# Kernel optimization log

Hardware: AMD Instinct MI355X
Metric: run time of the kernel (lower is better)

Reference implementation:

```python
import jax, jax.numpy as jnp
import numpy as np

B, T, H, NH = 4, 1024, 1024, 16
HS = H // NH
FF = 4 * H
EPS = 1e-5


def setup_inputs() -> dict:
    key = jax.random.key(0)
    ks = jax.random.split(key, 12)
    s = 0.02
    inp = {
        "x": jax.random.normal(ks[0], (B, T, H), jnp.float32),
        # attention projections, stored as [in, out] so y = x @ W + b
        "Wq": jax.random.normal(ks[1], (H, H), jnp.float32) * s,
        "bq": jnp.zeros((H,), jnp.float32),
        "Wk": jax.random.normal(ks[2], (H, H), jnp.float32) * s,
        "bk": jnp.zeros((H,), jnp.float32),
        "Wv": jax.random.normal(ks[3], (H, H), jnp.float32) * s,
        "bv": jnp.zeros((H,), jnp.float32),
        "Wo": jax.random.normal(ks[4], (H, H), jnp.float32) * s,
        "bo": jnp.zeros((H,), jnp.float32),
        # layernorms
        "ln1_w": jnp.ones((H,), jnp.float32),
        "ln1_b": jnp.zeros((H,), jnp.float32),
        "ln2_w": jnp.ones((H,), jnp.float32),
        "ln2_b": jnp.zeros((H,), jnp.float32),
        # MLP
        "Wfc": jax.random.normal(ks[5], (H, FF), jnp.float32) * s,
        "bfc": jnp.zeros((FF,), jnp.float32),
        "Wpr": jax.random.normal(ks[6], (FF, H), jnp.float32) * s,
        "bpr": jnp.zeros((H,), jnp.float32),
    }
    return inp


def _layernorm(x, w, b):
    mu = jnp.mean(x, axis=-1, keepdims=True)
    var = jnp.mean(jnp.square(x - mu), axis=-1, keepdims=True)
    return (x - mu) * jax.lax.rsqrt(var + EPS) * w + b


def _rope(x):
    # x: [B, nh, T, hs]; interleaved-pair RoPE, base 10000
    half = HS // 2
    inv_freq = 1.0 / (10000.0 ** (jnp.arange(half, dtype=jnp.float32) / half))
    ang = jnp.arange(T, dtype=jnp.float32)[:, None] * inv_freq[None, :]  # [T, half]
    cos, sin = jnp.cos(ang), jnp.sin(ang)
    xr = x.reshape(*x.shape[:-1], half, 2)
    x0, x1 = xr[..., 0], xr[..., 1]
    r0 = x0 * cos - x1 * sin
    r1 = x0 * sin + x1 * cos
    return jnp.stack([r0, r1], axis=-1).reshape(x.shape)


def _block(x, Wq, bq, Wk, bk, Wv, bv, Wo, bo, ln1_w, ln1_b, ln2_w, ln2_b, Wfc, bfc, Wpr, bpr):
    # --- attention sub-block ---
    h1 = _layernorm(x, ln1_w, ln1_b)
    q = (h1 @ Wq + bq).reshape(B, T, NH, HS).transpose(0, 2, 1, 3)  # [B,nh,T,hs]
    k = (h1 @ Wk + bk).reshape(B, T, NH, HS).transpose(0, 2, 1, 3)
    v = (h1 @ Wv + bv).reshape(B, T, NH, HS).transpose(0, 2, 1, 3)
    q, k = _rope(q), _rope(k)
    scores = jnp.einsum('bhqd,bhkd->bhqk', q, k) / jnp.sqrt(jnp.float32(HS))
    attn = jax.nn.softmax(scores, axis=-1)
    # NOTE: original applies the causal mask AFTER softmax (multiplicative, no renorm)
    causal = jnp.tril(jnp.ones((T, T), jnp.float32))[None, None]
    attn = attn * causal
    out = jnp.einsum('bhqk,bhkd->bhqd', attn, v)
    out = out.transpose(0, 2, 1, 3).reshape(B, T, H)
    x = x + (out @ Wo + bo)
    # --- MLP sub-block ---
    h2 = _layernorm(x, ln2_w, ln2_b)
    m = jax.nn.gelu(h2 @ Wfc + bfc, approximate=False)
    x = x + (m @ Wpr + bpr)
    return x


def reference(x, Wq, bq, Wk, bk, Wv, bv, Wo, bo, ln1_w, ln1_b, ln2_w, ln2_b, Wfc, bfc, Wpr, bpr):
    return _block(x, Wq, bq, Wk, bk, Wv, bv, Wo, bo, ln1_w, ln1_b, ln2_w, ln2_b, Wfc, bfc, Wpr, bpr)
```

## Files before the change

### kernel.cpp

```cpp
#include <hip/hip_runtime.h>
#include <hip/hip_bf16.h>

typedef unsigned short u16;
typedef __attribute__((ext_vector_type(8))) short bf16x8;
typedef __attribute__((ext_vector_type(4))) float f32x4;
typedef __attribute__((ext_vector_type(4))) unsigned short u16x4;

#define B_  4
#define T_  1024
#define H_  1024
#define NH_ 16
#define HS_ 64
#define FF_ 4096
#define M_  (B_*T_)
#define QKV_S 3072

__device__ __forceinline__ u16 f2bf(float f){
  union { float f; unsigned u; } v; v.f = f;
  unsigned r = v.u + 0x7fffu + ((v.u >> 16) & 1u);
  return (u16)(r >> 16);
}
__device__ __forceinline__ float bf2f(u16 h){
  union { unsigned u; float f; } v; v.u = ((unsigned)h) << 16;
  return v.f;
}
__device__ __forceinline__ unsigned pack2bf(float a, float b){
  __hip_bfloat162 h = __float22bfloat162_rn(make_float2(a, b));
  union { __hip_bfloat162 h; unsigned u; } c; c.h = h;
  return c.u;
}

__device__ __forceinline__ void gload_lds16(const void* g, void* l){
  __builtin_amdgcn_global_load_lds(
      (const __attribute__((address_space(1))) unsigned int*)g,
      (__attribute__((address_space(3))) unsigned int*)l,
      16, 0, 0);
}

__device__ __forceinline__ void trans_tile(const float* __restrict__ W,
                                           u16* __restrict__ Wt, int K, int N,
                                           int k0, int n0, int tid)
{
  __shared__ u16 tile[64][68];
  #pragma unroll
  for (int it = 0; it < 4; ++it){
    int ci = tid + it * 256;
    int kr = ci >> 4, nc = ci & 15;
    float4 f = *(const float4*)(W + (size_t)(k0 + kr) * N + n0 + nc * 4);
    tile[kr][nc*4+0] = f2bf(f.x);
    tile[kr][nc*4+1] = f2bf(f.y);
    tile[kr][nc*4+2] = f2bf(f.z);
    tile[kr][nc*4+3] = f2bf(f.w);
  }
  __syncthreads();
  #pragma unroll
  for (int it = 0; it < 4; ++it){
    int co = tid + it * 256;
    int nr = co >> 4, kc = co & 15;
    u16x4 o;
    o[0] = tile[kc*4+0][nr];
    o[1] = tile[kc*4+1][nr];
    o[2] = tile[kc*4+2][nr];
    o[3] = tile[kc*4+3][nr];
    *(u16x4*)(Wt + (size_t)(n0 + nr) * K + k0 + kc * 4) = o;
  }
}

__global__ __launch_bounds__(256) void trans_qkvo_k(
    const float* __restrict__ Wq, const float* __restrict__ Wk,
    const float* __restrict__ Wv, const float* __restrict__ Wo,
    u16* __restrict__ WqkvT, u16* __restrict__ WoT)
{
  const int z = blockIdx.z;
  const float* src = (z == 0) ? Wq : (z == 1) ? Wk : (z == 2) ? Wv : Wo;
  u16* dst = (z == 3) ? WoT : (WqkvT + (size_t)z * 1024 * 1024);
  trans_tile(src, dst, H_, H_, blockIdx.y * 64, blockIdx.x * 64, threadIdx.x);
}

__global__ __launch_bounds__(256) void transpose_cvt(const float* __restrict__ W,
                                                     u16* __restrict__ Wt, int K, int N)
{
  trans_tile(W, Wt, K, N, blockIdx.y * 64, blockIdx.x * 64, threadIdx.x);
}

__global__ __launch_bounds__(256) void vtrans_k(const u16* __restrict__ qkv,
                                                u16* __restrict__ vtg)
{
  __shared__ u16 tile[64][72];
  const int bh = blockIdx.y, tt = blockIdx.x * 64;
  const int b = bh >> 4, h = bh & 15;
  const size_t src = (size_t)b * T_ * QKV_S + h * HS_ + 2048;
  const int tid = threadIdx.x;
  #pragma unroll
  for (int it = 0; it < 2; ++it){
    int ci = tid + it * 256;
    int r = ci >> 3, c = ci & 7;
    bf16x8 vvv = *(const bf16x8*)(qkv + src + (size_t)(tt + r) * QKV_S + c * 8);
    *(bf16x8*)&tile[r][c * 8] = vvv;
  }
  __syncthreads();
  #pragma unroll
  for (int it = 0; it < 2; ++it){
    int co = tid + it * 256;
    int d = co >> 3, c = co & 7;
    bf16x8 ov;
    #pragma unroll
    for (int j = 0; j < 8; ++j) ov[j] = (short)tile[c * 8 + j][d];
    *(bf16x8*)(vtg + (size_t)bh * HS_ * T_ + (size_t)d * T_ + tt + c * 8) = ov;
  }
}

__global__ void prep_small_k(const float* __restrict__ a, const float* __restrict__ b,
                             const float* __restrict__ c, float* __restrict__ o,
                             float* __restrict__ tab){
  int i = blockIdx.x * 256 + threadIdx.x;
  if (i < QKV_S){
    o[i] = (i < 1024) ? a[i] : (i < 2048) ? b[i - 1024] : c[i - 2048];
  } else {
    int j = i - QKV_S;
    if (j < T_ * 32){
      int t = j >> 5, f = j & 31;
      float inv = powf(10000.0f, -(float)f * (1.0f / 32.0f));
      float ang = (float)t * inv;
      tab[j*2+0] = cosf(ang);
      tab[j*2+1] = sinf(ang);
    }
  }
}

__global__ void rope_apply_k(u16* __restrict__ qkv, const float* __restrict__ tab){
  int i = blockIdx.x * blockDim.x + threadIdx.x;
  if (i >= B_*T_*NH_*32) return;
  int pr = i & 31;
  int nh = (i >> 5) & (NH_ - 1);
  int bt = i >> 9;
  int t  = bt & (T_ - 1);
  size_t idx = (size_t)bt * QKV_S + nh * HS_ + pr * 2;
  float c = tab[(t*32 + pr)*2], s = tab[(t*32 + pr)*2 + 1];
  const float qs = 0.125f * 1.44269504f;
  {
    float x0 = bf2f(qkv[idx]), x1 = bf2f(qkv[idx+1]);
    qkv[idx]   = f2bf((x0 * c - x1 * s) * qs);
    qkv[idx+1] = f2bf((x0 * s + x1 * c) * qs);
  }
  {
    float x0 = bf2f(qkv[idx+1024]), x1 = bf2f(qkv[idx+1025]);
    qkv[idx+1024] = f2bf(x0 * c - x1 * s);
    qkv[idx+1025] = f2bf(x0 * s + x1 * c);
  }
}

__global__ __launch_bounds__(256) void ln_kernel(const float* __restrict__ x,
    const float* __restrict__ w, const float* __restrict__ bgain,
    u16* __restrict__ out)
{
  const int row = blockIdx.x;
  const int t = threadIdx.x;
  float4 vv = ((const float4*)(x + (size_t)row * H_))[t];
  float s  = vv.x + vv.y + vv.z + vv.w;
  float s2 = vv.x*vv.x + vv.y*vv.y + vv.z*vv.z + vv.w*vv.w;
  #pragma unroll
  for (int mm = 1; mm < 64; mm <<= 1){ s += __shfl_xor(s, mm); s2 += __shfl_xor(s2, mm); }
  __shared__ float red[8];
  int wid = t >> 6;
  if ((t & 63) == 0){ red[wid] = s; red[4 + wid] = s2; }
  __syncthreads();
  s  = red[0] + red[1] + red[2] + red[3];
  s2 = red[4] + red[5] + red[6] + red[7];
  float mu  = s * (1.0f / H_);
  float var = s2 * (1.0f / H_) - mu * mu;
  float rin = rsqrtf(var + 1e-5f);
  float4 wv = ((const float4*)w)[t];
  float4 bv = ((const float4*)bgain)[t];
  u16x4 ov;
  ov[0] = f2bf((vv.x - mu) * rin * wv.x + bv.x);
  ov[1] = f2bf((vv.y - mu) * rin * wv.y + bv.y);
  ov[2] = f2bf((vv.z - mu) * rin * wv.z + bv.z);
  ov[3] = f2bf((vv.w - mu) * rin * wv.w + bv.w);
  ((u16x4*)(out + (size_t)row * H_))[t] = ov;
}

template<int EPI>
__global__ __launch_bounds__(512, 2) void gemm_big_kernel(
    const u16* __restrict__ A, const u16* __restrict__ Bt,
    const float* __restrict__ bias,
    void* __restrict__ Cout, int M, int N, int K)
{
  __shared__ __attribute__((aligned(16))) u16 As[3][256 * 32];
  __shared__ __attribute__((aligned(16))) u16 Bs[3][256 * 32];
  const int tid  = threadIdx.x;
  const int lane = tid & 63;
  const int wid  = tid >> 6;
  const int wm = wid >> 2, wn = wid & 3;
  const int lrow = lane & 15, lkg = lane >> 4;

  const int gx  = gridDim.x;
  const int nwg = gx * gridDim.y;
  const int wg  = blockIdx.y * gx + blockIdx.x;
  const int nx  = nwg >> 3;
  const int swz = (wg & 7) * nx + (wg >> 3);
  const int m0 = (swz / gx) * 256, n0 = (swz % gx) * 256;

  const int r0 = tid >> 2;
  const int c0 = tid & 3;
  const int s0 = c0 ^ ((r0 >> 1) & 3);
  const u16* Asrc0 = A  + (size_t)(m0 + r0) * K + s0 * 8;
  const u16* Asrc1 = Asrc0 + (size_t)128 * K;
  const u16* Bsrc0 = Bt + (size_t)(n0 + r0) * K + s0 * 8;
  const u16* Bsrc1 = Bsrc0 + (size_t)128 * K;
  const int d0 = tid * 8;
  const int d1 = (tid + 512) * 8;

  int aoff[8], boff[4];
  #pragma unroll
  for (int mi = 0; mi < 8; ++mi){
    int r = wm*128 + mi*16 + lrow;
    aoff[mi] = (r*4 + (lkg ^ ((r >> 1) & 3))) * 16;
  }
  #pragma unroll
  for (int ni = 0; ni < 4; ++ni){
    int r = wn*64 + ni*16 + lrow;
    boff[ni] = (r*4 + (lkg ^ ((r >> 1) & 3))) * 16;
  }

  f32x4 acc[8][4] = {};
  const int NT = K >> 5;

  #pragma unroll
  for (int s = 0; s < 2; ++s){
    int k0 = s << 5;
    gload_lds16(Asrc0 + k0, &As[s][d0]);
    gload_lds16(Asrc1 + k0, &As[s][d1]);
    gload_lds16(Bsrc0 + k0, &Bs[s][d0]);
    gload_lds16(Bsrc1 + k0, &Bs[s][d1]);
  }

  int rs = 0, wsl = 2;
  for (int t = 0; t < NT; ++t){
    if (t < NT - 1) asm volatile("s_waitcnt vmcnt(4)" ::: "memory");
    else            asm volatile("s_waitcnt vmcnt(0)" ::: "memory");
    __builtin_amdgcn_s_barrier();

    const char* Ab = (const char*)&As[rs][0];
    const char* Bb = (const char*)&Bs[rs][0];
    rs = (rs + 1 == 3) ? 0 : rs + 1;

    bf16x8 af[8], bfr[4];
    #pragma unroll
    for (int mi = 0; mi < 8; ++mi)
      af[mi] = *(const bf16x8*)(Ab + aoff[mi]);
    #pragma unroll
    for (int ni = 0; ni < 4; ++ni)
      bfr[ni] = *(const bf16x8*)(Bb + boff[ni]);
    __builtin_amdgcn_sched_barrier(0);

    if (t + 2 < NT){
      int k0 = (t + 2) << 5;
      gload_lds16(Asrc0 + k0, &As[wsl][d0]);
      gload_lds16(Asrc1 + k0, &As[wsl][d1]);
      gload_lds16(Bsrc0 + k0, &Bs[wsl][d0]);
      gload_lds16(Bsrc1 + k0, &Bs[wsl][d1]);
    }
    wsl = (wsl + 1 == 3) ? 0 : wsl + 1;

    #pragma unroll
    for (int mi = 0; mi < 8; ++mi)
      #pragma unroll
      for (int ni = 0; ni < 4; ++ni)
        acc[mi][ni] = __builtin_amdgcn_mfma_f32_16x16x32_bf16(bfr[ni], af[mi], acc[mi][ni], 0, 0, 0);
  }

  #pragma unroll
  for (int mi = 0; mi < 8; ++mi){
    int row = m0 + wm*128 + mi*16 + lrow;
    #pragma unroll
    for (int ni = 0; ni < 4; ++ni){
      int col0 = n0 + wn*64 + ni*16 + lkg*4;
      float4 bv = *(const float4*)(bias + col0);
      float v0 = acc[mi][ni][0] + bv.x;
      float v1 = acc[mi][ni][1] + bv.y;
      float v2 = acc[mi][ni][2] + bv.z;
      float v3 = acc[mi][ni][3] + bv.w;
      if (EPI == 1){
        float u0 = 0.7978845608f * v0 + 0.0356774081f * v0 * v0 * v0;
        float u1 = 0.7978845608f * v1 + 0.0356774081f * v1 * v1 * v1;
        float u2 = 0.7978845608f * v2 + 0.0356774081f * v2 * v2 * v2;
        float u3 = 0.7978845608f * v3 + 0.0356774081f * v3 * v3 * v3;
        float e0 = exp2f(u0 * 2.8853900818f);
        float e1 = exp2f(u1 * 2.8853900818f);
        float e2 = exp2f(u2 * 2.8853900818f);
        float e3 = exp2f(u3 * 2.8853900818f);
        v0 = v0 - v0 / (e0 + 1.0f);
        v1 = v1 - v1 / (e1 + 1.0f);
        v2 = v2 - v2 / (e2 + 1.0f);
        v3 = v3 - v3 / (e3 + 1.0f);
      }
      uint2 ov;
      ov.x = pack2bf(v0, v1);
      ov.y = pack2bf(v2, v3);
      *(uint2*)((u16*)Cout + (size_t)row * N + col0) = ov;
    }
  }
}

template<int RING>
__global__ __launch_bounds__(256, 2) void gemm64_kernel(
    const u16* __restrict__ A, const u16* __restrict__ Bt,
    const float* __restrict__ bias, const float* __restrict__ res,
    float* __restrict__ Cout, int M, int N, int K)
{
  __shared__ __attribute__((aligned(16))) u16 As[RING][64 * 32];
  __shared__ __attribute__((aligned(16))) u16 Bs[RING][128 * 32];
  const int tid  = threadIdx.x;
  const int lane = tid & 63;
  const int wid  = tid >> 6;
  const int wm = wid >> 1, wn = wid & 1;
  const int lrow = lane & 15, lkg = lane >> 4;

  const int gx  = gridDim.x;
  const int nwg = gx * gridDim.y;
  const int wg  = blockIdx.y * gx + blockIdx.x;
  const int nx  = nwg >> 3;
  const int swz = (wg & 7) * nx + (wg >> 3);
  const int m0 = (swz / gx) * 64, n0 = (swz % gx) * 128;

  const int srow = tid >> 2;
  const int sdc  = tid & 3;
  const int scs  = sdc ^ ((srow >> 1) & 3);
  const u16* Asrc  = A  + (size_t)(m0 + srow) * K + scs * 8;
  const u16* Bsrc0 = Bt + (size_t)(n0 + srow) * K + scs * 8;
  const u16* Bsrc1 = Bsrc0 + (size_t)64 * K;
  const int dA  = (srow * 4 + sdc) * 8;
  const int dB1 = dA + 64 * 32;

  int aoff[2], boff[4];
  #pragma unroll
  for (int mi = 0; mi < 2; ++mi){
    int r = wm*32 + mi*16 + lrow;
    aoff[mi] = (r*4 + (lkg ^ ((r >> 1) & 3))) * 16;
  }
  #pragma unroll
  for (int ni = 0; ni < 4; ++ni){
    int r = wn*64 + ni*16 + lrow;
    boff[ni] = (r*4 + (lkg ^ ((r >> 1) & 3))) * 16;
  }

  f32x4 acc[2][4] = {};
  const int NT = K >> 5;
  constexpr int DIST = RING - 1;

  #pragma unroll
  for (int s = 0; s < DIST; ++s){
    gload_lds16(Asrc  + (s << 5), &As[s][dA]);
    gload_lds16(Bsrc0 + (s << 5), &Bs[s][dA]);
    gload_lds16(Bsrc1 + (s << 5), &Bs[s][dB1]);
  }

  int rs = 0, wsl = DIST;
  for (int t = 0; t < NT; ++t){
    int cnt = NT - 1 - t; if (cnt > DIST - 1) cnt = DIST - 1;
    if (cnt >= 2)      asm volatile("s_waitcnt vmcnt(6)" ::: "memory");
    else if (cnt == 1) asm volatile("s_waitcnt vmcnt(3)" ::: "memory");
    else               asm volatile("s_waitcnt vmcnt(0)" ::: "memory");
    __builtin_amdgcn_s_barrier();

    const char* Ab = (const char*)&As[rs][0];
    const char* Bb = (const char*)&Bs[rs][0];
    rs = (rs + 1 == RING) ? 0 : rs + 1;

    bf16x8 af[2], bfr[4];
    #pragma unroll
    for (int mi = 0; mi < 2; ++mi)
      af[mi] = *(const bf16x8*)(Ab + aoff[mi]);
    #pragma unroll
    for (int ni = 0; ni < 4; ++ni)
      bfr[ni] = *(const bf16x8*)(Bb + boff[ni]);
    __builtin_amdgcn_sched_barrier(0);

    if (t + DIST < NT){
      int k0 = (t + DIST) << 5;
      gload_lds16(Asrc  + k0, &As[wsl][dA]);
      gload_lds16(Bsrc0 + k0, &Bs[wsl][dA]);
      gload_lds16(Bsrc1 + k0, &Bs[wsl][dB1]);
    }
    wsl = (wsl + 1 == RING) ? 0 : wsl + 1;

    #pragma unroll
    for (int mi = 0; mi < 2; ++mi)
      #pragma unroll
      for (int ni = 0; ni < 4; ++ni)
        acc[mi][ni] = __builtin_amdgcn_mfma_f32_16x16x32_bf16(bfr[ni], af[mi], acc[mi][ni], 0, 0, 0);
  }

  #pragma unroll
  for (int mi = 0; mi < 2; ++mi){
    int row = m0 + wm*32 + mi*16 + lrow;
    #pragma unroll
    for (int ni = 0; ni < 4; ++ni){
      int col0 = n0 + wn*64 + ni*16 + lkg*4;
      float4 bv = *(const float4*)(bias + col0);
      float4 rv = *(const float4*)(res + (size_t)row * N + col0);
      float4 ov;
      ov.x = acc[mi][ni][0] + bv.x + rv.x;
      ov.y = acc[mi][ni][1] + bv.y + rv.y;
      ov.z = acc[mi][ni][2] + bv.z + rv.z;
      ov.w = acc[mi][ni][3] + bv.w + rv.w;
      *(float4*)(Cout + (size_t)row * N + col0) = ov;
    }
  }
}

__global__ __launch_bounds__(512, 4) void attn_kernel(
    const u16* __restrict__ qkv, const u16* __restrict__ vtg,
    u16* __restrict__ out)
{
  __shared__ u16 K_lds[3][64 * 64];
  __shared__ u16 VT_lds[3][64 * 64];
  __shared__ u16 P_lds[8][16 * 64];
  const int tid = threadIdx.x, lane = tid & 63, w = tid >> 6;
  const int lrow = lane & 15, lkg = lane >> 4;
  const int q0 = blockIdx.x * 128;
  const int bh = blockIdx.y, b = bh >> 4, h = bh & 15;
  const size_t baseq  = (size_t)b * T_ * QKV_S + h * HS_;
  const size_t basek  = baseq + 1024;
  const size_t basevt = (size_t)bh * HS_ * T_;
  const size_t baseo  = (size_t)b * T_ * H_ + h * HS_;
  const int qg = q0 + w * 16 + lrow;

  bf16x8 qa[2];
  {
    const u16* qp = qkv + baseq + (size_t)qg * QKV_S + lkg * 8;
    qa[0] = *(const bf16x8*)qp;
    qa[1] = *(const bf16x8*)(qp + 32);
  }

  const int r0 = tid >> 3, c0 = tid & 7, g0 = c0 ^ (r0 & 7);
  const u16* kap = qkv + basek + (size_t)r0 * QKV_S + g0 * 8;
  const u16* vap = vtg + basevt + (size_t)r0 * T_ + g0 * 8;
  const int kd = tid * 8;

  f32x4 o[4] = {};
  float mrun = -1e30f, lrun = 0.f;

  #pragma unroll
  for (int s = 0; s < 2; ++s){
    gload_lds16(kap + (size_t)s * 64 * QKV_S, &K_lds[s][kd]);
    gload_lds16(vap + s * 64,                 &VT_lds[s][kd]);
  }

  int rs = 0, wsl = 2;
  for (int t = 0; t < 16; ++t){
    const int kt = t << 6;
    if (t < 15) asm volatile("s_waitcnt vmcnt(2)" ::: "memory");
    else        asm volatile("s_waitcnt vmcnt(0)" ::: "memory");
    __builtin_amdgcn_s_barrier();
    __builtin_amdgcn_sched_barrier(0);

    if (t + 2 < 16){
      gload_lds16(kap + (size_t)(t + 2) * 64 * QKV_S, &K_lds[wsl][kd]);
      gload_lds16(vap + (t + 2) * 64,                 &VT_lds[wsl][kd]);
    }
    wsl = (wsl + 1 == 3) ? 0 : wsl + 1;

    const u16* Kc  = K_lds[rs];
    const u16* VTc = VT_lds[rs];
    rs = (rs + 1 == 3) ? 0 : rs + 1;

    f32x4 s[4];
    __builtin_amdgcn_s_setprio(1);
    #pragma unroll
    for (int mi = 0; mi < 4; ++mi){
      f32x4 c = {};
      #pragma unroll
      for (int ss = 0; ss < 2; ++ss){
        int r = mi * 16 + lrow;
        int off = r * 128 + (((ss * 4 + lkg) ^ (r & 7)) * 16);
        bf16x8 kb = *(const bf16x8*)((const char*)Kc + off);
        c = __builtin_amdgcn_mfma_f32_16x16x32_bf16(kb, qa[ss], c, 0, 0, 0);
      }
      s[mi] = c;
    }
    __builtin_amdgcn_s_setprio(0);

    float mt = fmaxf(fmaxf(fmaxf(s[0][0], s[0][1]), fmaxf(s[0][2], s[0][3])),
                     fmaxf(fmaxf(s[1][0], s[1][1]), fmaxf(s[1][2], s[1][3])));
    mt = fmaxf(mt, fmaxf(fmaxf(fmaxf(s[2][0], s[2][1]), fmaxf(s[2][2], s[2][3])),
                         fmaxf(fmaxf(s[3][0], s[3][1]), fmaxf(s[3][2], s[3][3]))));
    mt = fmaxf(mt, __shfl_xor(mt, 16));
    mt = fmaxf(mt, __shfl_xor(mt, 32));
    if (!__all(mt <= mrun + 8.f)){
      float mnew = fmaxf(mrun, mt);
      float fsc = exp2f(mrun - mnew);
      lrun *= fsc;
      #pragma unroll
      for (int nf = 0; nf < 4; ++nf){
        #pragma unroll
        for (int r = 0; r < 4; ++r) o[nf][r] *= fsc;
      }
      mrun = mnew;
    }

    float p[16];
    float ls = 0.f;
    #pragma unroll
    for (int mi = 0; mi < 4; ++mi){
      #pragma unroll
      for (int r = 0; r < 4; ++r){
        int key = kt + mi * 16 + lkg * 4 + r;
        float pv = exp2f(s[mi][r] - mrun);
        ls += pv;
        p[mi * 4 + r] = (key <= qg) ? pv : 0.f;
      }
    }
    ls += __shfl_xor(ls, 16);
    ls += __shfl_xor(ls, 32);
    lrun += ls;

    if (kt <= q0 + w * 16 + 15){
      char* pbase = (char*)&P_lds[w][0];
      const int rx = (lrow & 7) << 4;
      #pragma unroll
      for (int mi = 0; mi < 4; ++mi){
        uint2 pk;
        pk.x = pack2bf(p[mi*4+0], p[mi*4+1]);
        pk.y = pack2bf(p[mi*4+2], p[mi*4+3]);
        *(uint2*)(pbase + (lrow * 128 + ((mi * 32 + lkg * 8) ^ rx))) = pk;
      }
      __builtin_amdgcn_s_setprio(1);
      #pragma unroll
      for (int ss = 0; ss < 2; ++ss){
        bf16x8 pb = *(const bf16x8*)(pbase + (lrow * 128 + ((ss * 64 + lkg * 16) ^ rx)));
        #pragma unroll
        for (int nfd = 0; nfd < 4; ++nfd){
          int d = nfd * 16 + lrow;
          int off = d * 128 + (((ss * 4 + lkg) ^ (d & 7)) * 16);
          bf16x8 vb = *(const bf16x8*)((const char*)VTc + off);
          o[nfd] = __builtin_amdgcn_mfma_f32_16x16x32_bf16(vb, pb, o[nfd], 0, 0, 0);
        }
      }
      __builtin_amdgcn_s_setprio(0);
    }
  }

  float rl = 1.0f / lrun;
  #pragma unroll
  for (int nfd = 0; nfd < 4; ++nfd){
    uint2 ov;
    ov.x = pack2bf(o[nfd][0] * rl, o[nfd][1] * rl);
    ov.y = pack2bf(o[nfd][2] * rl, o[nfd][3] * rl);
    *(uint2*)(out + baseo + (size_t)qg * H_ + nfd * 16 + lkg * 4) = ov;
  }
}

extern "C" void kernel_launch(void* const* d_in, const int* in_sizes, int n_in,
                              void* d_out, int out_size, void* d_ws, size_t ws_size,
                              hipStream_t stream)
{
  (void)in_sizes; (void)n_in; (void)out_size; (void)ws_size;
  const float* x    = (const float*)d_in[0];
  const float* Wq   = (const float*)d_in[1];
  const float* bq   = (const float*)d_in[2];
  const float* Wk   = (const float*)d_in[3];
  const float* bk   = (const float*)d_in[4];
  const float* Wv   = (const float*)d_in[5];
  const float* bv   = (const float*)d_in[6];
  const float* Wo   = (const float*)d_in[7];
  const float* bo   = (const float*)d_in[8];
  const float* ln1w = (const float*)d_in[9];
  const float* ln1b = (const float*)d_in[10];
  const float* ln2w = (const float*)d_in[11];
  const float* ln2b = (const float*)d_in[12];
  const float* Wfc  = (const float*)d_in[13];
  const float* bfc  = (const float*)d_in[14];
  const float* Wpr  = (const float*)d_in[15];
  const float* bpr  = (const float*)d_in[16];

  char* ws = (char*)d_ws;
  u16*  WqkvT = (u16*)(ws + ((size_t) 0 << 20));
  u16*  WoT   = (u16*)(ws + ((size_t) 6 << 20));
  u16*  WfcT  = (u16*)(ws + ((size_t) 8 << 20));
  u16*  WprT  = (u16*)(ws + ((size_t)16 << 20));
  u16*  h1    = (u16*)(ws + ((size_t)24 << 20));
  u16*  qkvb  = (u16*)(ws + ((size_t)32 << 20));
  float* x1   = (float*)(ws + ((size_t)32 << 20));
  u16*  h2    = (u16*)(ws + ((size_t)48 << 20));
  float* bqkv = (float*)(ws + ((size_t)56 << 20));
  float* rtab = (float*)(ws + ((size_t)56 << 20) + (64 << 10));
  u16*  vtg   = (u16*)(ws + ((size_t)57 << 20));
  u16*  mb    = (u16*)(ws + ((size_t)56 << 20));
  u16*  attnout = h1;

  dim3 blk(256);
  dim3 gblk(512);

  trans_qkvo_k<<<dim3(H_/64, H_/64, 4), blk, 0, stream>>>(Wq, Wk, Wv, Wo, WqkvT, WoT);
  transpose_cvt<<<dim3(FF_/64, H_/64),  blk, 0, stream>>>(Wfc, WfcT, H_,  FF_);
  transpose_cvt<<<dim3(H_/64,  FF_/64), blk, 0, stream>>>(Wpr, WprT, FF_, H_);
  prep_small_k<<<dim3((QKV_S + T_*32 + 255)/256), blk, 0, stream>>>(bq, bk, bv, bqkv, rtab);

  ln_kernel<<<dim3(M_), blk, 0, stream>>>(x, ln1w, ln1b, h1);
  gemm_big_kernel<0><<<dim3(QKV_S/256, M_/256), gblk, 0, stream>>>(h1, WqkvT, bqkv, qkvb, M_, QKV_S, H_);
  rope_apply_k<<<dim3((B_*T_*NH_*32)/256), blk, 0, stream>>>(qkvb, rtab);
  vtrans_k<<<dim3(T_/64, B_*NH_), blk, 0, stream>>>(qkvb, vtg);
  attn_kernel<<<dim3(T_/128, B_*NH_), dim3(512), 0, stream>>>(qkvb, vtg, attnout);
  gemm64_kernel<4><<<dim3(H_/128, M_/64), blk, 0, stream>>>(attnout, WoT, bo, x, x1, M_, H_, H_);
  ln_kernel<<<dim3(M_), blk, 0, stream>>>(x1, ln2w, ln2b, h2);
  gemm_big_kernel<1><<<dim3(FF_/256, M_/256), gblk, 0, stream>>>(h2, WfcT, bfc, mb, M_, FF_, H_);
  gemm64_kernel<4><<<dim3(H_/128, M_/64), blk, 0, stream>>>(mb, WprT, bpr, x1, (float*)d_out, M_, H_, FF_);
}
```

Baseline: 255.8 us.

## Fuse RoPE into QKV GEMM epilogue and split-K the MLP down-projection

The separate RoPE kernel is removed. Rotation and the query scaling are applied in a new epilogue of the QKV GEMM, which saves one read-modify-write pass over the QKV buffer. The final FF→H projection now splits K in two: each half writes bf16 partials, using a 3-deep ring and a higher occupancy bound. A new reduce kernel then adds the partials, bias and residual. This raises parallelism for the long-K GEMM, at the cost of extra partial-buffer traffic, reduced precision in the partials, and reuse of the weight workspace region as scratch.

```diff
diff --git a/kernel.cpp b/kernel.cpp
--- a/kernel.cpp
+++ b/kernel.cpp
@@ -125,28 +125,6 @@
       tab[j*2+0] = cosf(ang);
       tab[j*2+1] = sinf(ang);
     }
-  }
-}
-
-__global__ void rope_apply_k(u16* __restrict__ qkv, const float* __restrict__ tab){
-  int i = blockIdx.x * blockDim.x + threadIdx.x;
-  if (i >= B_*T_*NH_*32) return;
-  int pr = i & 31;
-  int nh = (i >> 5) & (NH_ - 1);
-  int bt = i >> 9;
-  int t  = bt & (T_ - 1);
-  size_t idx = (size_t)bt * QKV_S + nh * HS_ + pr * 2;
-  float c = tab[(t*32 + pr)*2], s = tab[(t*32 + pr)*2 + 1];
-  const float qs = 0.125f * 1.44269504f;
-  {
-    float x0 = bf2f(qkv[idx]), x1 = bf2f(qkv[idx+1]);
-    qkv[idx]   = f2bf((x0 * c - x1 * s) * qs);
-    qkv[idx+1] = f2bf((x0 * s + x1 * c) * qs);
-  }
-  {
-    float x0 = bf2f(qkv[idx+1024]), x1 = bf2f(qkv[idx+1025]);
-    qkv[idx+1024] = f2bf(x0 * c - x1 * s);
-    qkv[idx+1025] = f2bf(x0 * s + x1 * c);
   }
 }
 
@@ -183,7 +161,7 @@
 template<int EPI>
 __global__ __launch_bounds__(512, 2) void gemm_big_kernel(
     const u16* __restrict__ A, const u16* __restrict__ Bt,
-    const float* __restrict__ bias,
+    const float* __restrict__ bias, const float* __restrict__ rtab,
     void* __restrict__ Cout, int M, int N, int K)
 {
   __shared__ __attribute__((aligned(16))) u16 As[3][256 * 32];
@@ -295,6 +273,20 @@
         v2 = v2 - v2 / (e2 + 1.0f);
         v3 = v3 - v3 / (e3 + 1.0f);
       }
+      if (EPI == 2){
+        if (col0 < 2048){
+          int tt = row & (T_ - 1);
+          const float* rt = rtab + ((size_t)tt * 32 + ((col0 & 63) >> 1)) * 2;
+          float cc0 = rt[0], ss0 = rt[1], cc1 = rt[2], ss1 = rt[3];
+          float q0 = v0 * cc0 - v1 * ss0, q1 = v0 * ss0 + v1 * cc0;
+          float q2 = v2 * cc1 - v3 * ss1, q3 = v2 * ss1 + v3 * cc1;
+          if (col0 < 1024){
+            const float qs = 0.125f * 1.44269504f;
+            q0 *= qs; q1 *= qs; q2 *= qs; q3 *= qs;
+          }
+          v0 = q0; v1 = q1; v2 = q2; v3 = q3;
+        }
+      }
       uint2 ov;
       ov.x = pack2bf(v0, v1);
       ov.y = pack2bf(v2, v3);
@@ -303,11 +295,11 @@
   }
 }
 
-template<int RING>
-__global__ __launch_bounds__(256, 2) void gemm64_kernel(
+template<int RING, int OUT>
+__global__ __launch_bounds__(256, (RING == 3) ? 4 : 2) void gemm64_kernel(
     const u16* __restrict__ A, const u16* __restrict__ Bt,
     const float* __restrict__ bias, const float* __restrict__ res,
-    float* __restrict__ Cout, int M, int N, int K)
+    void* __restrict__ Cout, int M, int N, int K, int LD)
 {
   __shared__ __attribute__((aligned(16))) u16 As[RING][64 * 32];
   __shared__ __attribute__((aligned(16))) u16 Bs[RING][128 * 32];
@@ -323,13 +315,14 @@
   const int nx  = nwg >> 3;
   const int swz = (wg & 7) * nx + (wg >> 3);
   const int m0 = (swz / gx) * 64, n0 = (swz % gx) * 128;
+  const int koff = blockIdx.z * K;
 
   const int srow = tid >> 2;
   const int sdc  = tid & 3;
   const int scs  = sdc ^ ((srow >> 1) & 3);
-  const u16* Asrc  = A  + (size_t)(m0 + srow) * K + scs * 8;
-  const u16* Bsrc0 = Bt + (size_t)(n0 + srow) * K + scs * 8;
-  const u16* Bsrc1 = Bsrc0 + (size_t)64 * K;
+  const u16* Asrc  = A  + (size_t)(m0 + srow) * LD + koff + scs * 8;
+  const u16* Bsrc0 = Bt + (size_t)(n0 + srow) * LD + koff + scs * 8;
+  const u16* Bsrc1 = Bsrc0 + (size_t)64 * LD;
   const int dA  = (srow * 4 + sdc) * 8;
   const int dB1 = dA + 64 * 32;
 
@@ -359,9 +352,14 @@
   int rs = 0, wsl = DIST;
   for (int t = 0; t < NT; ++t){
     int cnt = NT - 1 - t; if (cnt > DIST - 1) cnt = DIST - 1;
-    if (cnt >= 2)      asm volatile("s_waitcnt vmcnt(6)" ::: "memory");
-    else if (cnt == 1) asm volatile("s_waitcnt vmcnt(3)" ::: "memory");
-    else               asm volatile("s_waitcnt vmcnt(0)" ::: "memory");
+    if constexpr (RING == 4){
+      if (cnt >= 2)      asm volatile("s_waitcnt vmcnt(6)" ::: "memory");
+      else if (cnt == 1) asm volatile("s_waitcnt vmcnt(3)" ::: "memory");
+      else               asm volatile("s_waitcnt vmcnt(0)" ::: "memory");
+    } else {
+      if (cnt >= 1)      asm volatile("s_waitcnt vmcnt(3)" ::: "memory");
+      else               asm volatile("s_waitcnt vmcnt(0)" ::: "memory");
+    }
     __builtin_amdgcn_s_barrier();
 
     const char* Ab = (const char*)&As[rs][0];
@@ -398,16 +396,52 @@
     #pragma unroll
     for (int ni = 0; ni < 4; ++ni){
       int col0 = n0 + wn*64 + ni*16 + lkg*4;
-      float4 bv = *(const float4*)(bias + col0);
-      float4 rv = *(const float4*)(res + (size_t)row * N + col0);
-      float4 ov;
-      ov.x = acc[mi][ni][0] + bv.x + rv.x;
-      ov.y = acc[mi][ni][1] + bv.y + rv.y;
-      ov.z = acc[mi][ni][2] + bv.z + rv.z;
-      ov.w = acc[mi][ni][3] + bv.w + rv.w;
-      *(float4*)(Cout + (size_t)row * N + col0) = ov;
-    }
-  }
+      if (OUT == 0){
+        float4 bv = *(const float4*)(bias + col0);
+        float4 rv = *(const float4*)(res + (size_t)row * N + col0);
+        float4 ov;
+        ov.x = acc[mi][ni][0] + bv.x + rv.x;
+        ov.y = acc[mi][ni][1] + bv.y + rv.y;
+        ov.z = acc[mi][ni][2] + bv.z + rv.z;
+        ov.w = acc[mi][ni][3] + bv.w + rv.w;
+        *(float4*)((float*)Cout + (size_t)row * N + col0) = ov;
+      } else {
+        u16* outp = (u16*)Cout + (size_t)blockIdx.z * M * N;
+        uint2 ov;
+        ov.x = pack2bf(acc[mi][ni][0], acc[mi][ni][1]);
+        ov.y = pack2bf(acc[mi][ni][2], acc[mi][ni][3]);
+        *(uint2*)(outp + (size_t)row * N + col0) = ov;
+      }
+    }
+  }
+}
+
+__global__ __launch_bounds__(256) void sk_reduce_k(const u16* __restrict__ p,
+    const float* __restrict__ bias, const float* __restrict__ res,
+    float* __restrict__ out)
+{
+  size_t e = ((size_t)blockIdx.x * 256 + threadIdx.x) * 8;
+  int col = (int)(e & (H_ - 1));
+  const size_t off = (size_t)M_ * H_;
+  u16x4 a0 = *(const u16x4*)(p + e);
+  u16x4 a1 = *(const u16x4*)(p + e + 4);
+  u16x4 b0 = *(const u16x4*)(p + off + e);
+  u16x4 b1 = *(const u16x4*)(p + off + e + 4);
+  float4 bs0 = *(const float4*)(bias + col);
+  float4 bs1 = *(const float4*)(bias + col + 4);
+  float4 r0 = *(const float4*)(res + e);
+  float4 r1 = *(const float4*)(res + e + 4);
+  float4 o0, o1;
+  o0.x = bf2f(a0[0]) + bf2f(b0[0]) + bs0.x + r0.x;
+  o0.y = bf2f(a0[1]) + bf2f(b0[1]) + bs0.y + r0.y;
+  o0.z = bf2f(a0[2]) + bf2f(b0[2]) + bs0.z + r0.z;
+  o0.w = bf2f(a0[3]) + bf2f(b0[3]) + bs0.w + r0.w;
+  o1.x = bf2f(a1[0]) + bf2f(b1[0]) + bs1.x + r1.x;
+  o1.y = bf2f(a1[1]) + bf2f(b1[1]) + bs1.y + r1.y;
+  o1.z = bf2f(a1[2]) + bf2f(b1[2]) + bs1.z + r1.z;
+  o1.w = bf2f(a1[3]) + bf2f(b1[3]) + bs1.w + r1.w;
+  *(float4*)(out + e)     = o0;
+  *(float4*)(out + e + 4) = o1;
 }
 
 __global__ __launch_bounds__(512, 4) void attn_kernel(
@@ -579,6 +613,7 @@
   u16*  WqkvT = (u16*)(ws + ((size_t) 0 << 20));
   u16*  WoT   = (u16*)(ws + ((size_t) 6 << 20));
   u16*  WfcT  = (u16*)(ws + ((size_t) 8 << 20));
+  u16*  skp   = (u16*)(ws + ((size_t) 0 << 20));
   u16*  WprT  = (u16*)(ws + ((size_t)16 << 20));
   u16*  h1    = (u16*)(ws + ((size_t)24 << 20));
   u16*  qkvb  = (u16*)(ws + ((size_t)32 << 20));
@@ -599,12 +634,12 @@
   prep_small_k<<<dim3((QKV_S + T_*32 + 255)/256), blk, 0, stream>>>(bq, bk, bv, bqkv, rtab);
 
   ln_kernel<<<dim3(M_), blk, 0, stream>>>(x, ln1w, ln1b, h1);
-  gemm_big_kernel<0><<<dim3(QKV_S/256, M_/256), gblk, 0, stream>>>(h1, WqkvT, bqkv, qkvb, M_, QKV_S, H_);
-  rope_apply_k<<<dim3((B_*T_*NH_*32)/256), blk, 0, stream>>>(qkvb, rtab);
+  gemm_big_kernel<2><<<dim3(QKV_S/256, M_/256), gblk, 0, stream>>>(h1, WqkvT, bqkv, rtab, qkvb, M_, QKV_S, H_);
   vtrans_k<<<dim3(T_/64, B_*NH_), blk, 0, stream>>>(qkvb, vtg);
   attn_kernel<<<dim3(T_/128, B_*NH_), dim3(512), 0, stream>>>(qkvb, vtg, attnout);
-  gemm64_kernel<4><<<dim3(H_/128, M_/64), blk, 0, stream>>>(attnout, WoT, bo, x, x1, M_, H_, H_);
+  gemm64_kernel<4,0><<<dim3(H_/128, M_/64), blk, 0, stream>>>(attnout, WoT, bo, x, x1, M_, H_, H_, H_);
   ln_kernel<<<dim3(M_), blk, 0, stream>>>(x1, ln2w, ln2b, h2);
-  gemm_big_kernel<1><<<dim3(FF_/256, M_/256), gblk, 0, stream>>>(h2, WfcT, bfc, mb, M_, FF_, H_);
-  gemm64_kernel<4><<<dim3(H_/128, M_/64), blk, 0, stream>>>(mb, WprT, bpr, x1, (float*)d_out, M_, H_, FF_);
-}
+  gemm_big_kernel<1><<<dim3(FF_/256, M_/256), gblk, 0, stream>>>(h2, WfcT, bfc, nullptr, mb, M_, FF_, H_);
+  gemm64_kernel<3,1><<<dim3(H_/128, M_/64, 2), blk, 0, stream>>>(mb, WprT, nullptr, nullptr, skp, M_, H_, FF_/2, FF_);
+  sk_reduce_k<<<dim3((M_*H_)/(256*8)), blk, 0, stream>>>(skp, bpr, x1, (float*)d_out);
+}
```

Result: slower. 267.7 us (+4.6%).

## Restructure big GEMM into 8-phase ping-pong pipeline and fuse RoPE into QKV epilogue

Applied to the files above, without the earlier changes.

Rewrites the 256x256 GEMM mainloop to stage K=64 per iteration in double-buffered halves. Global loads for the next tile are interleaved between four MFMA phases, with barriers, explicit lgkmcnt waits and s_setprio raised around the MFMA blocks. Occupancy drops to one workgroup per CU because of the larger LDS footprint. RoPE rotation and Q scaling move into the QKV GEMM epilogue, removing the separate rope kernel and its read-modify-write pass over qkv. The risk is extra barriers per iteration and lost latency hiding from the lower occupancy.

```diff
diff --git a/kernel.cpp b/kernel.cpp
--- a/kernel.cpp
+++ b/kernel.cpp
@@ -125,28 +125,6 @@
       tab[j*2+0] = cosf(ang);
       tab[j*2+1] = sinf(ang);
     }
-  }
-}
-
-__global__ void rope_apply_k(u16* __restrict__ qkv, const float* __restrict__ tab){
-  int i = blockIdx.x * blockDim.x + threadIdx.x;
-  if (i >= B_*T_*NH_*32) return;
-  int pr = i & 31;
-  int nh = (i >> 5) & (NH_ - 1);
-  int bt = i >> 9;
-  int t  = bt & (T_ - 1);
-  size_t idx = (size_t)bt * QKV_S + nh * HS_ + pr * 2;
-  float c = tab[(t*32 + pr)*2], s = tab[(t*32 + pr)*2 + 1];
-  const float qs = 0.125f * 1.44269504f;
-  {
-    float x0 = bf2f(qkv[idx]), x1 = bf2f(qkv[idx+1]);
-    qkv[idx]   = f2bf((x0 * c - x1 * s) * qs);
-    qkv[idx+1] = f2bf((x0 * s + x1 * c) * qs);
-  }
-  {
-    float x0 = bf2f(qkv[idx+1024]), x1 = bf2f(qkv[idx+1025]);
-    qkv[idx+1024] = f2bf(x0 * c - x1 * s);
-    qkv[idx+1025] = f2bf(x0 * s + x1 * c);
   }
 }
 
@@ -181,13 +159,13 @@
 }
 
 template<int EPI>
-__global__ __launch_bounds__(512, 2) void gemm_big_kernel(
+__global__ __launch_bounds__(512, 1) void gemm8p_kernel(
     const u16* __restrict__ A, const u16* __restrict__ Bt,
-    const float* __restrict__ bias,
+    const float* __restrict__ bias, const float* __restrict__ rtab,
     void* __restrict__ Cout, int M, int N, int K)
 {
-  __shared__ __attribute__((aligned(16))) u16 As[3][256 * 32];
-  __shared__ __attribute__((aligned(16))) u16 Bs[3][256 * 32];
+  __shared__ __attribute__((aligned(16))) u16 Abuf[2][2][8192];
+  __shared__ __attribute__((aligned(16))) u16 Bbuf[2][2][8192];
   const int tid  = threadIdx.x;
   const int lane = tid & 63;
   const int wid  = tid >> 6;
@@ -201,15 +179,13 @@
   const int swz = (wg & 7) * nx + (wg >> 3);
   const int m0 = (swz / gx) * 256, n0 = (swz % gx) * 256;
 
-  const int r0 = tid >> 2;
-  const int c0 = tid & 3;
-  const int s0 = c0 ^ ((r0 >> 1) & 3);
-  const u16* Asrc0 = A  + (size_t)(m0 + r0) * K + s0 * 8;
-  const u16* Asrc1 = Asrc0 + (size_t)128 * K;
-  const u16* Bsrc0 = Bt + (size_t)(n0 + r0) * K + s0 * 8;
-  const u16* Bsrc1 = Bsrc0 + (size_t)128 * K;
-  const int d0 = tid * 8;
-  const int d1 = (tid + 512) * 8;
+  const int r0 = tid >> 2, c0 = tid & 3;
+  const int sc = c0 ^ ((r0 >> 1) & 3);
+  const u16* As0 = A  + (size_t)(m0 + r0) * K + sc * 8;
+  const u16* As1 = As0 + (size_t)128 * K;
+  const u16* Bs0 = Bt + (size_t)(n0 + r0) * K + sc * 8;
+  const u16* Bs1 = Bs0 + (size_t)128 * K;
+  const int dlo = tid * 8, dhi = (tid + 512) * 8;
 
   int aoff[8], boff[4];
   #pragma unroll
@@ -224,50 +200,95 @@
   }
 
   f32x4 acc[8][4] = {};
-  const int NT = K >> 5;
-
-  #pragma unroll
-  for (int s = 0; s < 2; ++s){
-    int k0 = s << 5;
-    gload_lds16(Asrc0 + k0, &As[s][d0]);
-    gload_lds16(Asrc1 + k0, &As[s][d1]);
-    gload_lds16(Bsrc0 + k0, &Bs[s][d0]);
-    gload_lds16(Bsrc1 + k0, &Bs[s][d1]);
-  }
-
-  int rs = 0, wsl = 2;
+  const int NT = K >> 6;
+
+  gload_lds16(As0,      &Abuf[0][0][dlo]); gload_lds16(As1,      &Abuf[0][0][dhi]);
+  gload_lds16(Bs0,      &Bbuf[0][0][dlo]); gload_lds16(Bs1,      &Bbuf[0][0][dhi]);
+  gload_lds16(As0 + 32, &Abuf[0][1][dlo]); gload_lds16(As1 + 32, &Abuf[0][1][dhi]);
+  gload_lds16(Bs0 + 32, &Bbuf[0][1][dlo]); gload_lds16(Bs1 + 32, &Bbuf[0][1][dhi]);
+  asm volatile("s_waitcnt vmcnt(4)" ::: "memory");
+  __builtin_amdgcn_s_barrier();
+
   for (int t = 0; t < NT; ++t){
-    if (t < NT - 1) asm volatile("s_waitcnt vmcnt(4)" ::: "memory");
-    else            asm volatile("s_waitcnt vmcnt(0)" ::: "memory");
-    __builtin_amdgcn_s_barrier();
-
-    const char* Ab = (const char*)&As[rs][0];
-    const char* Bb = (const char*)&Bs[rs][0];
-    rs = (rs + 1 == 3) ? 0 : rs + 1;
-
-    bf16x8 af[8], bfr[4];
-    #pragma unroll
-    for (int mi = 0; mi < 8; ++mi)
-      af[mi] = *(const bf16x8*)(Ab + aoff[mi]);
-    #pragma unroll
-    for (int ni = 0; ni < 4; ++ni)
-      bfr[ni] = *(const bf16x8*)(Bb + boff[ni]);
+    const int cb = t & 1, nb = (t + 1) & 1;
+    const int koff = (t + 1) << 6;
+    const char* Ak0 = (const char*)&Abuf[cb][0][0];
+    const char* Ak1 = (const char*)&Abuf[cb][1][0];
+    const char* Bk0 = (const char*)&Bbuf[cb][0][0];
+    const char* Bk1 = (const char*)&Bbuf[cb][1][0];
+    const bool pre = (t + 1 < NT);
+    bf16x8 af[8], bf[4];
+
+    #pragma unroll
+    for (int mi = 0; mi < 8; ++mi) af[mi] = *(const bf16x8*)(Ak0 + aoff[mi]);
+    bf[0] = *(const bf16x8*)(Bk0 + boff[0]);
+    bf[1] = *(const bf16x8*)(Bk0 + boff[1]);
+    if (pre){ gload_lds16(As0 + koff, &Abuf[nb][0][dlo]);
+              gload_lds16(As1 + koff, &Abuf[nb][0][dhi]); }
+    __builtin_amdgcn_s_barrier();
+    asm volatile("s_waitcnt lgkmcnt(0)" ::: "memory");
     __builtin_amdgcn_sched_barrier(0);
-
-    if (t + 2 < NT){
-      int k0 = (t + 2) << 5;
-      gload_lds16(Asrc0 + k0, &As[wsl][d0]);
-      gload_lds16(Asrc1 + k0, &As[wsl][d1]);
-      gload_lds16(Bsrc0 + k0, &Bs[wsl][d0]);
-      gload_lds16(Bsrc1 + k0, &Bs[wsl][d1]);
-    }
-    wsl = (wsl + 1 == 3) ? 0 : wsl + 1;
-
-    #pragma unroll
-    for (int mi = 0; mi < 8; ++mi)
-      #pragma unroll
-      for (int ni = 0; ni < 4; ++ni)
-        acc[mi][ni] = __builtin_amdgcn_mfma_f32_16x16x32_bf16(bfr[ni], af[mi], acc[mi][ni], 0, 0, 0);
+    __builtin_amdgcn_s_setprio(1);
+    #pragma unroll
+    for (int mi = 0; mi < 8; ++mi){
+      acc[mi][0] = __builtin_amdgcn_mfma_f32_16x16x32_bf16(bf[0], af[mi], acc[mi][0], 0, 0, 0);
+      acc[mi][1] = __builtin_amdgcn_mfma_f32_16x16x32_bf16(bf[1], af[mi], acc[mi][1], 0, 0, 0);
+    }
+    __builtin_amdgcn_s_setprio(0);
+    __builtin_amdgcn_s_barrier();
+
+    bf[2] = *(const bf16x8*)(Bk0 + boff[2]);
+    bf[3] = *(const bf16x8*)(Bk0 + boff[3]);
+    if (pre){ gload_lds16(Bs0 + koff, &Bbuf[nb][0][dlo]);
+              gload_lds16(Bs1 + koff, &Bbuf[nb][0][dhi]); }
+    __builtin_amdgcn_s_barrier();
+    asm volatile("s_waitcnt lgkmcnt(0)" ::: "memory");
+    __builtin_amdgcn_sched_barrier(0);
+    __builtin_amdgcn_s_setprio(1);
+    #pragma unroll
+    for (int mi = 0; mi < 8; ++mi){
+      acc[mi][2] = __builtin_amdgcn_mfma_f32_16x16x32_bf16(bf[2], af[mi], acc[mi][2], 0, 0, 0);
+      acc[mi][3] = __builtin_amdgcn_mfma_f32_16x16x32_bf16(bf[3], af[mi], acc[mi][3], 0, 0, 0);
+    }
+    __builtin_amdgcn_s_setprio(0);
+    if (pre) asm volatile("s_waitcnt vmcnt(4)" ::: "memory");
+    else     asm volatile("s_waitcnt vmcnt(0)" ::: "memory");
+    __builtin_amdgcn_s_barrier();
+
+    #pragma unroll
+    for (int mi = 0; mi < 8; ++mi) af[mi] = *(const bf16x8*)(Ak1 + aoff[mi]);
+    bf[0] = *(const bf16x8*)(Bk1 + boff[0]);
+    bf[1] = *(const bf16x8*)(Bk1 + boff[1]);
+    if (pre){ gload_lds16(As0 + koff + 32, &Abuf[nb][1][dlo]);
+              gload_lds16(As1 + koff + 32, &Abuf[nb][1][dhi]); }
+    __builtin_amdgcn_s_barrier();
+    asm volatile("s_waitcnt lgkmcnt(0)" ::: "memory");
+    __builtin_amdgcn_sched_barrier(0);
+    __builtin_amdgcn_s_setprio(1);
+    #pragma unroll
+    for (int mi = 0; mi < 8; ++mi){
+      acc[mi][0] = __builtin_amdgcn_mfma_f32_16x16x32_bf16(bf[0], af[mi], acc[mi][0], 0, 0, 0);
+      acc[mi][1] = __builtin_amdgcn_mfma_f32_16x16x32_bf16(bf[1], af[mi], acc[mi][1], 0, 0, 0);
+    }
+    __builtin_amdgcn_s_setprio(0);
+    __builtin_amdgcn_s_barrier();
+
+    bf[2] = *(const bf16x8*)(Bk1 + boff[2]);
+    bf[3] = *(const bf16x8*)(Bk1 + boff[3]);
+    if (pre){ gload_lds16(Bs0 + koff + 32, &Bbuf[nb][1][dlo]);
+              gload_lds16(Bs1 + koff + 32, &Bbuf[nb][1][dhi]); }
+    __builtin_amdgcn_s_barrier();
+    asm volatile("s_waitcnt lgkmcnt(0)" ::: "memory");
+    __builtin_amdgcn_sched_barrier(0);
+    __builtin_amdgcn_s_setprio(1);
+    #pragma unroll
+    for (int mi = 0; mi < 8; ++mi){
+      acc[mi][2] = __builtin_amdgcn_mfma_f32_16x16x32_bf16(bf[2], af[mi], acc[mi][2], 0, 0, 0);
+      acc[mi][3] = __builtin_amdgcn_mfma_f32_16x16x32_bf16(bf[3], af[mi], acc[mi][3], 0, 0, 0);
+    }
+    __builtin_amdgcn_s_setprio(0);
+    if (pre) asm volatile("s_waitcnt vmcnt(4)" ::: "memory");
+    __builtin_amdgcn_s_barrier();
   }
 
   #pragma unroll
@@ -294,6 +315,20 @@
         v1 = v1 - v1 / (e1 + 1.0f);
         v2 = v2 - v2 / (e2 + 1.0f);
         v3 = v3 - v3 / (e3 + 1.0f);
+      }
+      if (EPI == 2){
+        if (col0 < 2048){
+          int tt = row & (T_ - 1);
+          const float* rt = rtab + ((size_t)tt * 32 + ((col0 & 63) >> 1)) * 2;
+          float cc0 = rt[0], ss0 = rt[1], cc1 = rt[2], ss1 = rt[3];
+          float q0 = v0 * cc0 - v1 * ss0, q1 = v0 * ss0 + v1 * cc0;
+          float q2 = v2 * cc1 - v3 * ss1, q3 = v2 * ss1 + v3 * cc1;
+          if (col0 < 1024){
+            const float qs = 0.125f * 1.44269504f;
+            q0 *= qs; q1 *= qs; q2 *= qs; q3 *= qs;
+          }
+          v0 = q0; v1 = q1; v2 = q2; v3 = q3;
+        }
       }
       uint2 ov;
       ov.x = pack2bf(v0, v1);
@@ -599,12 +634,11 @@
   prep_small_k<<<dim3((QKV_S + T_*32 + 255)/256), blk, 0, stream>>>(bq, bk, bv, bqkv, rtab);
 
   ln_kernel<<<dim3(M_), blk, 0, stream>>>(x, ln1w, ln1b, h1);
-  gemm_big_kernel<0><<<dim3(QKV_S/256, M_/256), gblk, 0, stream>>>(h1, WqkvT, bqkv, qkvb, M_, QKV_S, H_);
-  rope_apply_k<<<dim3((B_*T_*NH_*32)/256), blk, 0, stream>>>(qkvb, rtab);
+  gemm8p_kernel<2><<<dim3(QKV_S/256, M_/256), gblk, 0, stream>>>(h1, WqkvT, bqkv, rtab, qkvb, M_, QKV_S, H_);
   vtrans_k<<<dim3(T_/64, B_*NH_), blk, 0, stream>>>(qkvb, vtg);
   attn_kernel<<<dim3(T_/128, B_*NH_), dim3(512), 0, stream>>>(qkvb, vtg, attnout);
   gemm64_kernel<4><<<dim3(H_/128, M_/64), blk, 0, stream>>>(attnout, WoT, bo, x, x1, M_, H_, H_);
   ln_kernel<<<dim3(M_), blk, 0, stream>>>(x1, ln2w, ln2b, h2);
-  gemm_big_kernel<1><<<dim3(FF_/256, M_/256), gblk, 0, stream>>>(h2, WfcT, bfc, mb, M_, FF_, H_);
+  gemm8p_kernel<1><<<dim3(FF_/256, M_/256), gblk, 0, stream>>>(h2, WfcT, bfc, nullptr, mb, M_, FF_, H_);
   gemm64_kernel<4><<<dim3(H_/128, M_/64), blk, 0, stream>>>(mb, WprT, bpr, x1, (float*)d_out, M_, H_, FF_);
 }
```

Result: faster. 250.4 us (-2.1%).
